# Kernel tuning notes

Hardware: AMD Instinct MI355X
Metric: run time of the kernel (lower is better)

The kernel has to match this reference:

```python
import jax, jax.numpy as jnp
import numpy as np

MAXLEN = 20
ALPHA = 0.5
B = 16384
D = 1024


def setup_inputs() -> dict:
    key = jax.random.key(0)
    k_in, k_len = jax.random.split(key)
    x = jax.random.normal(k_in, (B, MAXLEN, D), dtype=jnp.float32)
    # per-session valid lengths in [1, MAXLEN]; valid tokens are the FIRST L positions
    lengths = jax.random.randint(k_len, (B,), 1, MAXLEN + 1)
    mask = (jnp.arange(MAXLEN)[None, :] < lengths[:, None]).astype(jnp.int32)
    return {"input": x, "mask": mask}


def reference(input, mask):
    # seq_len[i] = number of valid tokens (first L positions of row i)
    lengths = jnp.sum(mask, axis=1)  # [B] int32
    t = jnp.arange(MAXLEN, dtype=jnp.int32)[None, :]  # [1, S]
    valid = t < lengths[:, None]  # [B, S]
    # original takes weight[maxlen-L:] = [alpha^(L-1), ..., alpha^0] aligned to tokens 0..L-1
    expo = (lengths[:, None] - 1 - t).astype(jnp.float32)  # [B, S]
    w = jnp.where(valid, jnp.power(jnp.float32(ALPHA), expo), 0.0)  # [B, S]
    w = w / jnp.sum(w, axis=1, keepdims=True)
    # weighted pooling: [B, S] x [B, S, D] -> [B, D]
    return jnp.einsum("bs,bsd->bd", w, input)
```

## Files before the change

kernel.cpp:

```cpp
#include <hip/hip_runtime.h>

#define MAXLEN 20
#define DIM 1024
#define NB 16384

__global__ __launch_bounds__(256) void tdap_kernel(
    const float* __restrict__ x,
    const int*   __restrict__ mask,
    float*       __restrict__ out)
{
    const int b   = blockIdx.x;
    const int tid = threadIdx.x;

    int L = 0;
#pragma unroll
    for (int t = 0; t < MAXLEN; ++t) L += mask[b * MAXLEN + t];

    const float inv_norm = 1.0f / (2.0f * (1.0f - ldexpf(1.0f, -L)));
    float w = ldexpf(1.0f, -(L - 1)) * inv_norm;

    const float4* xp = reinterpret_cast<const float4*>(x + (size_t)b * MAXLEN * DIM) + tid;
    float4 acc = make_float4(0.f, 0.f, 0.f, 0.f);

    for (int t = 0; t < L; ++t) {
        float4 v = xp[(size_t)t * (DIM / 4)];
        acc.x = fmaf(w, v.x, acc.x);
        acc.y = fmaf(w, v.y, acc.y);
        acc.z = fmaf(w, v.z, acc.z);
        acc.w = fmaf(w, v.w, acc.w);
        w *= 2.0f;
    }

    reinterpret_cast<float4*>(out + (size_t)b * DIM)[tid] = acc;
}

extern "C" void kernel_launch(void* const* d_in, const int* in_sizes, int n_in,
                              void* d_out, int out_size, void* d_ws, size_t ws_size,
                              hipStream_t stream) {
    const float* x    = (const float*)d_in[0];
    const int*   mask = (const int*)d_in[1];
    float*       out  = (float*)d_out;
    tdap_kernel<<<NB, 256, 0, stream>>>(x, mask, out);
}
```

Before: 160.7 us.

## Unroll token loop by four with nontemporal loads and vectorized mask read

Issues the first token's load before computing the length, reads the mask row as five int4 vectors, and unrolls the token loop by four with independent accumulators so several loads are in flight at once. Loads and the output store use nontemporal hints, and launch bounds request 8 blocks per SM. The point is to raise memory-level parallelism in this bandwidth-bound pooling. The four accumulators are combined with power-of-two scaling, which changes floating-point summation order slightly.

```diff
diff --git a/kernel.cpp b/kernel.cpp
--- a/kernel.cpp
+++ b/kernel.cpp
@@ -4,7 +4,10 @@
 #define DIM 1024
 #define NB 16384
 
-__global__ __launch_bounds__(256) void tdap_kernel(
+typedef float vf4 __attribute__((ext_vector_type(4)));
+typedef int   vi4 __attribute__((ext_vector_type(4)));
+
+__global__ __launch_bounds__(256, 8) void tdap_kernel(
     const float* __restrict__ x,
     const int*   __restrict__ mask,
     float*       __restrict__ out)
@@ -12,26 +15,48 @@
     const int b   = blockIdx.x;
     const int tid = threadIdx.x;
 
-    int L = 0;
-#pragma unroll
-    for (int t = 0; t < MAXLEN; ++t) L += mask[b * MAXLEN + t];
+    const vf4* xp = reinterpret_cast<const vf4*>(x + (size_t)b * MAXLEN * DIM) + tid;
+
+    vf4 v0 = __builtin_nontemporal_load(&xp[0]);
+
+    const vi4* mrow = reinterpret_cast<const vi4*>(mask + (size_t)b * MAXLEN);
+    vi4 m0 = mrow[0], m1 = mrow[1], m2 = mrow[2], m3 = mrow[3], m4 = mrow[4];
+    const int L = m0.x + m0.y + m0.z + m0.w
+                + m1.x + m1.y + m1.z + m1.w
+                + m2.x + m2.y + m2.z + m2.w
+                + m3.x + m3.y + m3.z + m3.w
+                + m4.x + m4.y + m4.z + m4.w;
 
     const float inv_norm = 1.0f / (2.0f * (1.0f - ldexpf(1.0f, -L)));
     float w = ldexpf(1.0f, -(L - 1)) * inv_norm;
 
-    const float4* xp = reinterpret_cast<const float4*>(x + (size_t)b * MAXLEN * DIM) + tid;
-    float4 acc = make_float4(0.f, 0.f, 0.f, 0.f);
+    vf4 a0 = w * v0;
+    vf4 a1 = (vf4)0.0f;
+    vf4 a2 = (vf4)0.0f;
+    vf4 a3 = (vf4)0.0f;
 
-    for (int t = 0; t < L; ++t) {
-        float4 v = xp[(size_t)t * (DIM / 4)];
-        acc.x = fmaf(w, v.x, acc.x);
-        acc.y = fmaf(w, v.y, acc.y);
-        acc.z = fmaf(w, v.z, acc.z);
-        acc.w = fmaf(w, v.w, acc.w);
+    int t = 1;
+    w *= 2.0f;
+    for (; t + 4 <= L; t += 4) {
+        vf4 u0 = __builtin_nontemporal_load(&xp[(size_t)(t + 0) * (DIM / 4)]);
+        vf4 u1 = __builtin_nontemporal_load(&xp[(size_t)(t + 1) * (DIM / 4)]);
+        vf4 u2 = __builtin_nontemporal_load(&xp[(size_t)(t + 2) * (DIM / 4)]);
+        vf4 u3 = __builtin_nontemporal_load(&xp[(size_t)(t + 3) * (DIM / 4)]);
+        a0 += w * u0;
+        a1 += w * u1;
+        a2 += w * u2;
+        a3 += w * u3;
+        w *= 16.0f;
+    }
+    for (; t < L; ++t) {
+        vf4 u = __builtin_nontemporal_load(&xp[(size_t)t * (DIM / 4)]);
+        a0 += w * u;
         w *= 2.0f;
     }
 
-    reinterpret_cast<float4*>(out + (size_t)b * DIM)[tid] = acc;
+    vf4 acc = a0 + 2.0f * a1 + 4.0f * a2 + 8.0f * a3;
+
+    __builtin_nontemporal_store(acc, reinterpret_cast<vf4*>(out + (size_t)b * DIM) + tid);
 }
 
 extern "C" void kernel_launch(void* const* d_in, const int* in_sizes, int n_in,
```

Result: faster. 141.5 us (median of 2 runs) (-12.0%).
